# Performance work log

Hardware: AMD Instinct MI355X
Metric: run time of the kernel (lower is better)

## Reference

```python
import jax, jax.numpy as jnp
import numpy as np

N_SRC, N_DST, E = 50000, 50000, 800000
D_GT, D_AG = 64, 64
HID, HEADS = 256, 4
FPH = HID // HEADS  # 64
N_ACT = 16
NEG_SLOPE = 0.2  # DGL GATv2Conv default negative_slope


def setup_inputs() -> dict:
    key = jax.random.key(0)
    ks = jax.random.split(key, 16)
    f32 = jnp.float32
    return {
        "feat_gt": jax.random.normal(ks[0], (N_SRC, D_GT), f32),
        "feat_agent": jax.random.normal(ks[1], (N_DST, D_AG), f32),
        "h0": jax.random.normal(ks[2], (N_DST, HID), f32),
        "edge_src": jax.random.randint(ks[3], (E,), 0, N_SRC),
        "edge_dst": jax.random.randint(ks[4], (E,), 0, N_DST),
        "W_src": jax.random.normal(ks[5], (D_GT, HID), f32) * 0.1,
        "b_src": jnp.zeros((HID,), f32),
        "W_dst": jax.random.normal(ks[6], (D_AG, HID), f32) * 0.1,
        "b_dst": jnp.zeros((HID,), f32),
        "attn": jax.random.normal(ks[7], (HEADS, FPH), f32) * 0.1,
        "W_res": jax.random.normal(ks[8], (D_AG, HID), f32) * 0.1,
        "b_res": jnp.zeros((HID,), f32),
        "W_ih": jax.random.normal(ks[9], (3 * HID, HID), f32) * 0.05,
        "W_hh": jax.random.normal(ks[10], (3 * HID, HID), f32) * 0.05,
        "b_ih": jnp.zeros((3 * HID,), f32),
        "b_hh": jnp.zeros((3 * HID,), f32),
        "W_out": jax.random.normal(ks[11], (HID, N_ACT), f32) * 0.05,
        "b_out": jnp.zeros((N_ACT,), f32),
    }


def _gatv2(feat_gt, feat_agent, edge_src, edge_dst,
           W_src, b_src, W_dst, b_dst, attn, W_res, b_res):
    # GATv2Conv (bipartite, share_weights=False, residual=True, activation=ReLU)
    fs = (feat_gt @ W_src + b_src).reshape(N_SRC, HEADS, FPH)    # [Ns,H,F]
    fd = (feat_agent @ W_dst + b_dst).reshape(N_DST, HEADS, FPH)  # [Nd,H,F]
    e = fs[edge_src] + fd[edge_dst]                               # [E,H,F]
    e = jnp.where(e > 0, e, NEG_SLOPE * e)                        # LeakyReLU
    score = jnp.einsum('ehf,hf->eh', e, attn)                     # [E,H]
    # edge softmax segmented by destination node
    smax = jax.lax.stop_gradient(
        jax.ops.segment_max(score, edge_dst, num_segments=N_DST))  # [Nd,H]
    ex = jnp.exp(score - smax[edge_dst])
    den = jax.ops.segment_sum(ex, edge_dst, num_segments=N_DST)   # [Nd,H]
    alpha = ex / den[edge_dst]                                    # [E,H]
    msg = alpha[:, :, None] * fs[edge_src]                        # [E,H,F]
    rst = jax.ops.segment_sum(msg, edge_dst, num_segments=N_DST)  # [Nd,H,F]
    rst = rst.reshape(N_DST, HID) + (feat_agent @ W_res + b_res)  # residual
    return jax.nn.relu(rst)


def _gru_cell(x, h, W_ih, W_hh, b_ih, b_hh):
    gi = x @ W_ih.T + b_ih
    gh = h @ W_hh.T + b_hh
    ir, iz, inn = jnp.split(gi, 3, axis=-1)
    hr, hz, hn = jnp.split(gh, 3, axis=-1)
    r = jax.nn.sigmoid(ir + hr)
    z = jax.nn.sigmoid(iz + hz)
    n = jnp.tanh(inn + r * hn)
    return (1.0 - z) * n + z * h


def reference(feat_gt, feat_agent, h0, edge_src, edge_dst,
              W_src, b_src, W_dst, b_dst, attn, W_res, b_res,
              W_ih, W_hh, b_ih, b_hh, W_out, b_out):
    x = _gatv2(feat_gt, feat_agent, edge_src, edge_dst,
               W_src, b_src, W_dst, b_dst, attn, W_res, b_res)  # [Nd,HID]
    h = _gru_cell(x, h0, W_ih, W_hh, b_ih, b_hh)                # [Nd,HID]
    logits = h @ W_out + b_out                                  # [Nd,N_ACT]
    return (logits, h)
```

## Files before the change

### kernel.cpp

```cpp
#include <hip/hip_runtime.h>
#include <stdint.h>

#define N_SRCN 50000
#define N_DSTN 50000
#define NE     800000
#define HIDN   256
#define NEG    0.2f

typedef __attribute__((ext_vector_type(8)))  short short8;
typedef __attribute__((ext_vector_type(16))) float float16v;

__device__ __forceinline__ float bf2f(unsigned short u){
    union { unsigned u32; float f; } c; c.u32 = ((unsigned)u) << 16; return c.f;
}
__device__ __forceinline__ unsigned short f2bf(float f){
    union { float f; unsigned u; } c; c.f = f;
    unsigned r = c.u + 0x7fffu + ((c.u >> 16) & 1u);
    return (unsigned short)(r >> 16);
}
__device__ __forceinline__ float4 ld4b(const unsigned short* p){
    uint2 u = *reinterpret_cast<const uint2*>(p);
    float4 r;
    r.x = bf2f((unsigned short)(u.x & 0xffff));
    r.y = bf2f((unsigned short)(u.x >> 16));
    r.z = bf2f((unsigned short)(u.y & 0xffff));
    r.w = bf2f((unsigned short)(u.y >> 16));
    return r;
}

__global__ void pack_kernel(const float* __restrict__ Wsrc, const float* __restrict__ Wdst,
                            const float* __restrict__ Wres, const float* __restrict__ Wih,
                            const float* __restrict__ Whh,
                            unsigned short* __restrict__ Wt2,
                            unsigned short* __restrict__ Wf){
    int i = blockIdx.x * 256 + threadIdx.x;
    if (i < 49152){
        int which = i >> 14, j = i & 16383;
        int k = j >> 8, c = j & 255;
        const float* W = (which == 0) ? Wsrc : (which == 1 ? Wdst : Wres);
        float v = W[j];
        int off = which * 16384 + (c >> 5) * 2048 + (k >> 4) * 512
                + (((k >> 3) & 1) * 32 + (c & 31)) * 8 + (k & 7);
        Wt2[off] = f2bf(v);
    } else if (i < 49152 + 196608){
        int o = i - 49152;
        int row = o >> 8, k = o & 255;
        int g = row >> 8, c = row & 255;
        float v = Wih[o];
        int off = g * 131072 + (c >> 5) * 16384 + (k >> 4) * 512
                + (((k >> 3) & 1) * 32 + (c & 31)) * 8 + (k & 7);
        Wf[off] = f2bf(v);
    } else if (i < 49152 + 393216){
        int o = i - 49152 - 196608;
        int row = o >> 8, k = o & 255;
        int g = row >> 8, c = row & 255;
        float v = Whh[o];
        int off = g * 131072 + (c >> 5) * 16384 + (16 + (k >> 4)) * 512
                + (((k >> 3) & 1) * 32 + (c & 31)) * 8 + (k & 7);
        Wf[off] = f2bf(v);
    }
}

__global__ __launch_bounds__(256) void proj_kernel(
        const float* __restrict__ Agt, const float* __restrict__ Aag,
        const unsigned short* __restrict__ Wt2,
        const float* __restrict__ bsrc, const float* __restrict__ bdst,
        const float* __restrict__ bres,
        unsigned short* __restrict__ fs, unsigned short* __restrict__ fd,
        unsigned short* __restrict__ resb){
    __shared__ unsigned short As[64 * 72];
    __shared__ unsigned short Cs[64 * 72];
    int z = blockIdx.z;
    const float* A = (z == 0) ? Agt : Aag;
    const float* bias = (z == 0) ? bsrc : (z == 1 ? bdst : bres);
    unsigned short* out = (z == 0) ? fs : (z == 1 ? fd : resb);
    const unsigned short* Wb = Wt2 + z * 16384;
    int tid = threadIdx.x;
    int m0 = blockIdx.y * 64;
    #pragma unroll
    for (int i = 0; i < 4; ++i){
        int ci = tid + i * 256;
        int row = ci >> 4;
        int k4 = (ci & 15) << 2;
        int gr = m0 + row; if (gr >= N_SRCN) gr = N_SRCN - 1;
        float4 v = *reinterpret_cast<const float4*>(A + (size_t)gr * 64 + k4);
        unsigned short* dp = As + row * 72 + k4;
        dp[0] = f2bf(v.x); dp[1] = f2bf(v.y); dp[2] = f2bf(v.z); dp[3] = f2bf(v.w);
    }
    __syncthreads();
    int lane = tid & 63, w = tid >> 6;
    int l31 = lane & 31, half = lane >> 5;
    int msub = (w & 1) * 32;
    int cbw = blockIdx.x * 2 + (w >> 1);
    const unsigned short* bb = Wb + cbw * 2048 + lane * 8;
    const unsigned short* ap = As + (msub + l31) * 72 + half * 8;
    float16v acc = {0,0,0,0,0,0,0,0,0,0,0,0,0,0,0,0};
    #pragma unroll
    for (int ks = 0; ks < 4; ++ks){
        short8 a = *reinterpret_cast<const short8*>(ap + ks * 16);
        short8 b = *reinterpret_cast<const short8*>(bb + ks * 512);
        acc = __builtin_amdgcn_mfma_f32_32x32x16_bf16(a, b, acc, 0, 0, 0);
    }
    float bv = bias[cbw * 32 + l31];
    int ccol = (w >> 1) * 32 + l31;
    #pragma unroll
    for (int r = 0; r < 16; ++r){
        int row = (r & 3) + 8 * (r >> 2) + 4 * half + msub;
        Cs[row * 72 + ccol] = f2bf(acc[r] + bv);
    }
    __syncthreads();
    int srow = tid >> 2, chunk = tid & 3;
    int gr2 = m0 + srow;
    if (gr2 < N_SRCN){
        const uint4* sp = reinterpret_cast<const uint4*>(Cs + srow * 72 + chunk * 16);
        uint4* gp = reinterpret_cast<uint4*>(out + (size_t)gr2 * 256 + blockIdx.x * 64 + chunk * 16);
        gp[0] = sp[0];
        gp[1] = sp[1];
    }
}

__global__ void degree_kernel(const int* __restrict__ dst, int* __restrict__ deg){
    int i = blockIdx.x * 256 + threadIdx.x;
    if (i < NE) atomicAdd(&deg[dst[i]], 1);
}

__global__ void scan1_kernel(const int* __restrict__ deg, int* __restrict__ bsum){
    __shared__ int s[256];
    int tid = threadIdx.x;
    int i = blockIdx.x * 256 + tid;
    s[tid] = (i < N_DSTN) ? deg[i] : 0;
    __syncthreads();
    #pragma unroll
    for (int off = 128; off; off >>= 1){
        if (tid < off) s[tid] += s[tid + off];
        __syncthreads();
    }
    if (tid == 0) bsum[blockIdx.x] = s[0];
}

__global__ void scan2_kernel(const int* __restrict__ bsum, int* __restrict__ boff){
    __shared__ int s[256];
    int tid = threadIdx.x;
    int v = (tid < 196) ? bsum[tid] : 0;
    s[tid] = v;
    __syncthreads();
    #pragma unroll
    for (int off = 1; off < 256; off <<= 1){
        int t = (tid >= off) ? s[tid - off] : 0;
        __syncthreads();
        s[tid] += t;
        __syncthreads();
    }
    if (tid < 196) boff[tid] = s[tid] - v;
}

__global__ void scan3_kernel(const int* __restrict__ deg, const int* __restrict__ boff,
                             int* __restrict__ ptr, int* __restrict__ cursor){
    __shared__ int s[256];
    int tid = threadIdx.x;
    int i = blockIdx.x * 256 + tid;
    int v = (i < N_DSTN) ? deg[i] : 0;
    s[tid] = v;
    __syncthreads();
    #pragma unroll
    for (int off = 1; off < 256; off <<= 1){
        int t = (tid >= off) ? s[tid - off] : 0;
        __syncthreads();
        s[tid] += t;
        __syncthreads();
    }
    int ex = s[tid] - v + boff[blockIdx.x];
    if (i < N_DSTN){ ptr[i] = ex; cursor[i] = ex; }
}

__global__ void scatter_kernel(const int* __restrict__ src, const int* __restrict__ dst,
                               int* __restrict__ cursor, int* __restrict__ csr){
    int i = blockIdx.x * 256 + threadIdx.x;
    if (i < NE){
        int d = dst[i];
        int pos = atomicAdd(&cursor[d], 1);
        csr[pos] = src[i];
    }
}

__global__ __launch_bounds__(256) void aggregate_kernel(
        const unsigned short* __restrict__ fs, const unsigned short* __restrict__ fd,
        const unsigned short* __restrict__ res, const float* __restrict__ attn,
        const int* __restrict__ ptr, const int* __restrict__ deg,
        const int* __restrict__ csr, unsigned short* __restrict__ x){
    int wv = threadIdx.x >> 6;
    int d = blockIdx.x * 4 + wv;
    if (d >= N_DSTN) return;
    int lane = threadIdx.x & 63;
    int c4 = lane * 4;
    float4 fdv = ld4b(fd + (size_t)d * 256 + c4);
    float4 at = *reinterpret_cast<const float4*>(attn + (lane >> 4) * 64 + (lane & 15) * 4);
    int p = ptr[d], dg = deg[d];
    float l = 0.f;
    float4 acc = make_float4(0.f, 0.f, 0.f, 0.f);
    for (int base = 0; base < dg; base += 64){
        int cnt = min(64, dg - base);
        int sreg = (lane < cnt) ? csr[p + base + lane] : 0;
        float4 b0 = ld4b(fs + (size_t)__shfl(sreg, 0) * 256 + c4);
        float4 b1 = ld4b(fs + (size_t)__shfl(sreg, 1 & 63) * 256 + c4);
        float4 b2 = ld4b(fs + (size_t)__shfl(sreg, 2 & 63) * 256 + c4);
        float4 b3 = ld4b(fs + (size_t)__shfl(sreg, 3 & 63) * 256 + c4);
        for (int j = 0; j < cnt; j += 4){
            float4 n0 = ld4b(fs + (size_t)__shfl(sreg, (j + 4) & 63) * 256 + c4);
            float4 n1 = ld4b(fs + (size_t)__shfl(sreg, (j + 5) & 63) * 256 + c4);
            float4 n2 = ld4b(fs + (size_t)__shfl(sreg, (j + 6) & 63) * 256 + c4);
            float4 n3 = ld4b(fs + (size_t)__shfl(sreg, (j + 7) & 63) * 256 + c4);
#define PROC(BV, T) { \
            float ex = BV.x + fdv.x; ex = ex > 0.f ? ex : NEG * ex; \
            float ey = BV.y + fdv.y; ey = ey > 0.f ? ey : NEG * ey; \
            float ez = BV.z + fdv.z; ez = ez > 0.f ? ez : NEG * ez; \
            float ew = BV.w + fdv.w; ew = ew > 0.f ? ew : NEG * ew; \
            float part = ex * at.x + ey * at.y + ez * at.z + ew * at.w; \
            part += __shfl_xor(part, 1); \
            part += __shfl_xor(part, 2); \
            part += __shfl_xor(part, 4); \
            part += __shfl_xor(part, 8); \
            float wgt = ((j + (T)) < cnt) ? __expf(part) : 0.f; \
            l += wgt; \
            acc.x = fmaf(wgt, BV.x, acc.x); \
            acc.y = fmaf(wgt, BV.y, acc.y); \
            acc.z = fmaf(wgt, BV.z, acc.z); \
            acc.w = fmaf(wgt, BV.w, acc.w); }
            PROC(b0, 0) PROC(b1, 1) PROC(b2, 2) PROC(b3, 3)
#undef PROC
            b0 = n0; b1 = n1; b2 = n2; b3 = n3;
        }
    }
    float inv = (l > 0.f) ? 1.f / l : 0.f;
    float4 rv = ld4b(res + (size_t)d * 256 + c4);
    float xx = fmaxf(fmaf(acc.x, inv, rv.x), 0.f);
    float xy = fmaxf(fmaf(acc.y, inv, rv.y), 0.f);
    float xz = fmaxf(fmaf(acc.z, inv, rv.z), 0.f);
    float xw = fmaxf(fmaf(acc.w, inv, rv.w), 0.f);
    uint2 o;
    o.x = (unsigned)f2bf(xx) | ((unsigned)f2bf(xy) << 16);
    o.y = (unsigned)f2bf(xz) | ((unsigned)f2bf(xw) << 16);
    *reinterpret_cast<uint2*>(x + (size_t)d * 256 + c4) = o;
}

__global__ __launch_bounds__(1024, 4) void gru_kernel(
        const unsigned short* __restrict__ Xb,
        const float* __restrict__ H0, const unsigned short* __restrict__ Wf,
        const float* __restrict__ bih, const float* __restrict__ bhh,
        float* __restrict__ outH){
    __shared__ unsigned short As[64 * 512];
    int tid = threadIdx.x;
    int m0 = blockIdx.x << 6;
    #pragma unroll
    for (int i = 0; i < 2; ++i){
        int ci = tid + i * 1024;
        int row = ci >> 5, c = ci & 31;
        int gr = m0 + row; if (gr >= N_DSTN) gr = N_DSTN - 1;
        *reinterpret_cast<uint4*>(As + row * 512 + ((c ^ (row & 7)) << 3)) =
            *reinterpret_cast<const uint4*>(Xb + (size_t)gr * 256 + (c << 3));
    }
    #pragma unroll
    for (int i = 0; i < 2; ++i){
        int ci = tid + i * 1024;
        int row = ci >> 5, c = ci & 31;
        int gr = m0 + row; if (gr >= N_DSTN) gr = N_DSTN - 1;
        const float* hp = H0 + (size_t)gr * 256 + (c << 3);
        float4 f0 = *reinterpret_cast<const float4*>(hp);
        float4 f1 = *reinterpret_cast<const float4*>(hp + 4);
        uint4 o;
        o.x = (unsigned)f2bf(f0.x) | ((unsigned)f2bf(f0.y) << 16);
        o.y = (unsigned)f2bf(f0.z) | ((unsigned)f2bf(f0.w) << 16);
        o.z = (unsigned)f2bf(f1.x) | ((unsigned)f2bf(f1.y) << 16);
        o.w = (unsigned)f2bf(f1.z) | ((unsigned)f2bf(f1.w) << 16);
        *reinterpret_cast<uint4*>(As + row * 512 + (((c + 32) ^ (row & 7)) << 3)) = o;
    }
    __syncthreads();
    int w = tid >> 6, lane = tid & 63;
    int l31 = lane & 31, half = lane >> 5;
    int rt = w >> 3, ct = w & 7;
    int arow = rt * 32 + l31;
    int rl = arow & 7;
    const unsigned short* apb = As + arow * 512;
    const unsigned short* br = Wf + (size_t)ct * 16384 + lane * 8;
    const unsigned short* bz = br + 131072;
    const unsigned short* bn = br + 262144;
    float16v zv = {0,0,0,0,0,0,0,0,0,0,0,0,0,0,0,0};
    float16v ar = zv, az = zv, anx = zv, anh = zv;
    #pragma unroll
    for (int kk = 0; kk < 16; ++kk){
        short8 a  = *reinterpret_cast<const short8*>(apb + (((kk * 2 + half) ^ rl) << 3));
        short8 vr = *reinterpret_cast<const short8*>(br + kk * 512);
        short8 vz = *reinterpret_cast<const short8*>(bz + kk * 512);
        short8 vn = *reinterpret_cast<const short8*>(bn + kk * 512);
        ar  = __builtin_amdgcn_mfma_f32_32x32x16_bf16(a, vr, ar,  0, 0, 0);
        az  = __builtin_amdgcn_mfma_f32_32x32x16_bf16(a, vz, az,  0, 0, 0);
        anx = __builtin_amdgcn_mfma_f32_32x32x16_bf16(a, vn, anx, 0, 0, 0);
    }
    #pragma unroll
    for (int kk = 16; kk < 32; ++kk){
        short8 a  = *reinterpret_cast<const short8*>(apb + (((kk * 2 + half) ^ rl) << 3));
        short8 vr = *reinterpret_cast<const short8*>(br + kk * 512);
        short8 vz = *reinterpret_cast<const short8*>(bz + kk * 512);
        short8 vn = *reinterpret_cast<const short8*>(bn + kk * 512);
        ar  = __builtin_amdgcn_mfma_f32_32x32x16_bf16(a, vr, ar,  0, 0, 0);
        az  = __builtin_amdgcn_mfma_f32_32x32x16_bf16(a, vz, az,  0, 0, 0);
        anh = __builtin_amdgcn_mfma_f32_32x32x16_bf16(a, vn, anh, 0, 0, 0);
    }
    int cg = ct * 32 + l31;
    float rb = bih[cg] + bhh[cg];
    float zb = bih[256 + cg] + bhh[256 + cg];
    float bin = bih[512 + cg], bhn = bhh[512 + cg];
    #pragma unroll
    for (int r = 0; r < 16; ++r){
        int m = m0 + rt * 32 + (r & 3) + 8 * (r >> 2) + 4 * half;
        if (m < N_DSTN){
            float h0v = H0[(size_t)m * 256 + cg];
            float rrg = 1.f / (1.f + __expf(-(ar[r] + rb)));
            float zg  = 1.f / (1.f + __expf(-(az[r] + zb)));
            float nx = anx[r] + bin + rrg * (anh[r] + bhn);
            float tm = __expf(-2.f * fabsf(nx));
            float nn = (1.f - tm) / (1.f + tm);
            nn = (nx >= 0.f) ? nn : -nn;
            outH[(size_t)m * 256 + cg] = (1.f - zg) * nn + zg * h0v;
        }
    }
}

__global__ __launch_bounds__(256) void logits_kernel(
        const float* __restrict__ H, const float* __restrict__ Wout,
        const float* __restrict__ bout, float* __restrict__ outL){
    __shared__ float Hl[16 * 260];
    __shared__ float Wl[16 * 260];
    int tid = threadIdx.x;
    int m0 = blockIdx.x * 16;
    #pragma unroll
    for (int i = 0; i < 4; ++i){
        int ci = tid + i * 256;
        int row = ci >> 6;
        int c4 = (ci & 63) << 2;
        int gr = m0 + row; if (gr >= N_DSTN) gr = N_DSTN - 1;
        float4 v = *reinterpret_cast<const float4*>(H + (size_t)gr * 256 + c4);
        float* dp = Hl + row * 260 + c4;
        dp[0] = v.x; dp[1] = v.y; dp[2] = v.z; dp[3] = v.w;
    }
    #pragma unroll
    for (int i = 0; i < 16; ++i){
        int ci = tid + i * 256;
        int c = ci >> 4, j = ci & 15;
        Wl[j * 260 + c] = Wout[c * 16 + j];
    }
    __syncthreads();
    int row = tid >> 4, j = tid & 15;
    const float* hr = Hl + row * 260;
    const float* wr = Wl + j * 260;
    float acc = bout[j];
    #pragma unroll
    for (int c = 0; c < 256; c += 4){
        float4 hv = *reinterpret_cast<const float4*>(hr + c);
        float4 wv = *reinterpret_cast<const float4*>(wr + c);
        acc = fmaf(hv.x, wv.x, fmaf(hv.y, wv.y, fmaf(hv.z, wv.z, fmaf(hv.w, wv.w, acc))));
    }
    int m = m0 + row;
    if (m < N_DSTN) outL[m * 16 + j] = acc;
}

extern "C" void kernel_launch(void* const* d_in, const int* in_sizes, int n_in,
                              void* d_out, int out_size, void* d_ws, size_t ws_size,
                              hipStream_t stream){
    const float* feat_gt = (const float*)d_in[0];
    const float* feat_ag = (const float*)d_in[1];
    const float* h0      = (const float*)d_in[2];
    const int*   e_src   = (const int*)d_in[3];
    const int*   e_dst   = (const int*)d_in[4];
    const float* W_src   = (const float*)d_in[5];
    const float* b_src   = (const float*)d_in[6];
    const float* W_dst   = (const float*)d_in[7];
    const float* b_dst   = (const float*)d_in[8];
    const float* attn    = (const float*)d_in[9];
    const float* W_res   = (const float*)d_in[10];
    const float* b_res   = (const float*)d_in[11];
    const float* W_ih    = (const float*)d_in[12];
    const float* W_hh    = (const float*)d_in[13];
    const float* b_ih    = (const float*)d_in[14];
    const float* b_hh    = (const float*)d_in[15];
    const float* W_out   = (const float*)d_in[16];
    const float* b_out   = (const float*)d_in[17];

    float* outL = (float*)d_out;
    float* outH = outL + (size_t)N_DSTN * 16;

    char* ws = (char*)d_ws;
    size_t off = 0;
    auto alloc = [&](size_t bytes) -> void* {
        void* p = ws + off; off = (off + bytes + 255) & ~(size_t)255; return p;
    };
    unsigned short* fs   = (unsigned short*)alloc((size_t)N_SRCN * 256 * 2);
    unsigned short* fd   = (unsigned short*)alloc((size_t)N_DSTN * 256 * 2);
    unsigned short* res  = (unsigned short*)alloc((size_t)N_DSTN * 256 * 2);
    unsigned short* xb   = (unsigned short*)alloc((size_t)N_DSTN * 256 * 2);
    unsigned short* Wt2  = (unsigned short*)alloc(49152 * 2);
    unsigned short* Wf   = (unsigned short*)alloc(393216 * 2);
    int* deg    = (int*)alloc(N_DSTN * 4);
    int* ptr    = (int*)alloc(N_DSTN * 4);
    int* cursor = (int*)alloc(N_DSTN * 4);
    int* csr    = (int*)alloc((size_t)NE * 4);
    int* bsum   = (int*)alloc(256 * 4);
    int* boff   = (int*)alloc(256 * 4);

    hipMemsetAsync(deg, 0, N_DSTN * 4, stream);
    pack_kernel<<<1728, 256, 0, stream>>>(W_src, W_dst, W_res, W_ih, W_hh, Wt2, Wf);

    proj_kernel<<<dim3(4, 782, 3), 256, 0, stream>>>(feat_gt, feat_ag, Wt2,
                                                     b_src, b_dst, b_res, fs, fd, res);

    degree_kernel<<<3125, 256, 0, stream>>>(e_dst, deg);
    scan1_kernel<<<196, 256, 0, stream>>>(deg, bsum);
    scan2_kernel<<<1, 256, 0, stream>>>(bsum, boff);
    scan3_kernel<<<196, 256, 0, stream>>>(deg, boff, ptr, cursor);
    scatter_kernel<<<3125, 256, 0, stream>>>(e_src, e_dst, cursor, csr);
    aggregate_kernel<<<12500, 256, 0, stream>>>(fs, fd, res, attn, ptr, deg, csr, xb);

    gru_kernel<<<782, 1024, 0, stream>>>(xb, h0, Wf, b_ih, b_hh, outH);
    logits_kernel<<<3125, 256, 0, stream>>>(outH, W_out, b_out, outL);
}
```

Baseline: 486.8 us.

## Stage GRU weight tiles in LDS with double-buffered global_load_lds

The GRU kernel now cooperatively copies each k-step slice of the r/z/n weight tiles into a double-buffered shared-memory array using direct global-to-LDS loads. Previously each wave read its B fragments straight from global memory, so the two row-tile waves fetched the same weights twice. The change aims to cut those duplicate loads and overlap the next slice's fetch with the current MFMAs. In exchange it adds a block-wide barrier on each of the 32 k-steps and about 48 KB more LDS per block, which may lower occupancy. It also relies on the async LDS writes being finished by the time the barrier releases.

```diff
diff --git a/kernel.cpp b/kernel.cpp
--- a/kernel.cpp
+++ b/kernel.cpp
@@ -26,6 +26,12 @@
     r.z = bf2f((unsigned short)(u.y & 0xffff));
     r.w = bf2f((unsigned short)(u.y >> 16));
     return r;
+}
+__device__ __forceinline__ void gload_lds16(const unsigned short* g, unsigned short* l){
+    __builtin_amdgcn_global_load_lds(
+        (const __attribute__((address_space(1))) void*)g,
+        (__attribute__((address_space(3))) void*)l,
+        16, 0, 0);
 }
 
 __global__ void pack_kernel(const float* __restrict__ Wsrc, const float* __restrict__ Wdst,
@@ -249,8 +255,10 @@
         const float* __restrict__ bih, const float* __restrict__ bhh,
         float* __restrict__ outH){
     __shared__ unsigned short As[64 * 512];
+    __shared__ unsigned short Bs[2 * 12288];
     int tid = threadIdx.x;
     int m0 = blockIdx.x << 6;
+    int w = tid >> 6, lane = tid & 63;
     #pragma unroll
     for (int i = 0; i < 2; ++i){
         int ci = tid + i * 1024;
@@ -274,37 +282,42 @@
         o.w = (unsigned)f2bf(f1.z) | ((unsigned)f2bf(f1.w) << 16);
         *reinterpret_cast<uint4*>(As + row * 512 + (((c + 32) ^ (row & 7)) << 3)) = o;
     }
-    __syncthreads();
-    int w = tid >> 6, lane = tid & 63;
+    {
+        int g = w >> 3, cb = w & 7;
+        gload_lds16(Wf + g * 131072 + cb * 16384 + lane * 8, Bs + w * 512);
+        if (w < 8)
+            gload_lds16(Wf + 2 * 131072 + w * 16384 + lane * 8, Bs + (16 + w) * 512);
+    }
+    __syncthreads();
+
     int l31 = lane & 31, half = lane >> 5;
     int rt = w >> 3, ct = w & 7;
     int arow = rt * 32 + l31;
     int rl = arow & 7;
     const unsigned short* apb = As + arow * 512;
-    const unsigned short* br = Wf + (size_t)ct * 16384 + lane * 8;
-    const unsigned short* bz = br + 131072;
-    const unsigned short* bn = br + 262144;
+    int sg = w >> 3, scb = w & 7;
     float16v zv = {0,0,0,0,0,0,0,0,0,0,0,0,0,0,0,0};
     float16v ar = zv, az = zv, anx = zv, anh = zv;
-    #pragma unroll
-    for (int kk = 0; kk < 16; ++kk){
-        short8 a  = *reinterpret_cast<const short8*>(apb + (((kk * 2 + half) ^ rl) << 3));
-        short8 vr = *reinterpret_cast<const short8*>(br + kk * 512);
-        short8 vz = *reinterpret_cast<const short8*>(bz + kk * 512);
-        short8 vn = *reinterpret_cast<const short8*>(bn + kk * 512);
-        ar  = __builtin_amdgcn_mfma_f32_32x32x16_bf16(a, vr, ar,  0, 0, 0);
-        az  = __builtin_amdgcn_mfma_f32_32x32x16_bf16(a, vz, az,  0, 0, 0);
-        anx = __builtin_amdgcn_mfma_f32_32x32x16_bf16(a, vn, anx, 0, 0, 0);
-    }
-    #pragma unroll
-    for (int kk = 16; kk < 32; ++kk){
-        short8 a  = *reinterpret_cast<const short8*>(apb + (((kk * 2 + half) ^ rl) << 3));
-        short8 vr = *reinterpret_cast<const short8*>(br + kk * 512);
-        short8 vz = *reinterpret_cast<const short8*>(bz + kk * 512);
-        short8 vn = *reinterpret_cast<const short8*>(bn + kk * 512);
-        ar  = __builtin_amdgcn_mfma_f32_32x32x16_bf16(a, vr, ar,  0, 0, 0);
-        az  = __builtin_amdgcn_mfma_f32_32x32x16_bf16(a, vz, az,  0, 0, 0);
-        anh = __builtin_amdgcn_mfma_f32_32x32x16_bf16(a, vn, anh, 0, 0, 0);
+    #pragma unroll 2
+    for (int p = 0; p < 32; ++p){
+        if (p + 1 < 32){
+            unsigned short* db = Bs + ((p + 1) & 1) * 12288;
+            gload_lds16(Wf + sg * 131072 + scb * 16384 + (p + 1) * 512 + lane * 8,
+                        db + w * 512);
+            if (w < 8)
+                gload_lds16(Wf + 2 * 131072 + w * 16384 + (p + 1) * 512 + lane * 8,
+                            db + (16 + w) * 512);
+        }
+        const unsigned short* bp = Bs + (p & 1) * 12288;
+        short8 a  = *reinterpret_cast<const short8*>(apb + (((p * 2 + half) ^ rl) << 3));
+        short8 vr = *reinterpret_cast<const short8*>(bp + (0 * 8 + ct) * 512 + lane * 8);
+        short8 vz = *reinterpret_cast<const short8*>(bp + (1 * 8 + ct) * 512 + lane * 8);
+        short8 vn = *reinterpret_cast<const short8*>(bp + (2 * 8 + ct) * 512 + lane * 8);
+        ar = __builtin_amdgcn_mfma_f32_32x32x16_bf16(a, vr, ar, 0, 0, 0);
+        az = __builtin_amdgcn_mfma_f32_32x32x16_bf16(a, vz, az, 0, 0, 0);
+        if (p < 16) anx = __builtin_amdgcn_mfma_f32_32x32x16_bf16(a, vn, anx, 0, 0, 0);
+        else        anh = __builtin_amdgcn_mfma_f32_32x32x16_bf16(a, vn, anh, 0, 0, 0);
+        __syncthreads();
     }
     int cg = ct * 32 + l31;
     float rb = bih[cg] + bhh[cg];
```

Result: faster. 458.5 us (-5.8%).
